# Performance work log

Measured on AMD Instinct MI355X. Metric: run time of the kernel, lower is better.

## Reference

```python
import jax, jax.numpy as jnp
import numpy as np

N_NODES = 100000
N_EDGES = 400000
N_GRAPHS = 4096
IN_DIM = 128
HID = 64
HEADS = 8
NEG_SLOPE = 0.2


def setup_inputs() -> dict:
    key = jax.random.key(0)
    ks = jax.random.split(key, 12)
    x = jax.random.normal(ks[0], (N_NODES, IN_DIM), dtype=jnp.float32)
    edge_index = jax.random.randint(ks[1], (2, N_EDGES), 0, N_NODES, dtype=jnp.int64)
    batch = jnp.sort(jax.random.randint(ks[2], (N_NODES,), 0, N_GRAPHS, dtype=jnp.int64))
    s = 1.0 / np.sqrt(IN_DIM)
    W1 = jax.random.normal(ks[3], (IN_DIM, HEADS * HID), dtype=jnp.float32) * s
    att_src1 = jax.random.normal(ks[4], (HEADS, HID), dtype=jnp.float32) * 0.1
    att_dst1 = jax.random.normal(ks[5], (HEADS, HID), dtype=jnp.float32) * 0.1
    b1 = jnp.zeros((HEADS * HID,), dtype=jnp.float32)
    s2 = 1.0 / np.sqrt(HEADS * HID)
    W2 = jax.random.normal(ks[6], (HEADS * HID, HID), dtype=jnp.float32) * s2
    att_src2 = jax.random.normal(ks[7], (1, HID), dtype=jnp.float32) * 0.1
    att_dst2 = jax.random.normal(ks[8], (1, HID), dtype=jnp.float32) * 0.1
    b2 = jnp.zeros((HID,), dtype=jnp.float32)
    Wf = jax.random.normal(ks[9], (HID, 1), dtype=jnp.float32) * (1.0 / np.sqrt(HID))
    bf = jnp.zeros((1,), dtype=jnp.float32)
    return {"x": x, "edge_index": edge_index, "batch": batch,
            "W1": W1, "att_src1": att_src1, "att_dst1": att_dst1, "b1": b1,
            "W2": W2, "att_src2": att_src2, "att_dst2": att_dst2, "b2": b2,
            "Wf": Wf, "bf": bf}


def _gat_layer(x, src, dst, W, att_src, att_dst, bias, heads, out_ch, concat):
    # PyG GATConv math (add_self_loops handled by caller via src/dst)
    n = x.shape[0]
    h = (x @ W).reshape(n, heads, out_ch)          # [N, H, C]
    a_s = (h * att_src[None]).sum(-1)               # [N, H]
    a_d = (h * att_dst[None]).sum(-1)               # [N, H]
    alpha = a_s[src] + a_d[dst]                     # [E, H]
    alpha = jax.nn.leaky_relu(alpha, NEG_SLOPE)
    amax = jax.ops.segment_max(alpha, dst, num_segments=n)
    alpha = jnp.exp(alpha - amax[dst])
    denom = jax.ops.segment_sum(alpha, dst, num_segments=n)
    alpha = alpha / (denom[dst] + 1e-16)
    msg = h[src] * alpha[:, :, None]                # [E, H, C]
    out = jax.ops.segment_sum(msg, dst, num_segments=n)  # [N, H, C]
    out = out.reshape(n, heads * out_ch) if concat else out.mean(axis=1)
    return out + bias


def reference(x, edge_index, batch, W1, att_src1, att_dst1, b1,
              W2, att_src2, att_dst2, b2, Wf, bf):
    n = x.shape[0]
    loop = jnp.arange(n, dtype=edge_index.dtype)
    src = jnp.concatenate([edge_index[0], loop])
    dst = jnp.concatenate([edge_index[1], loop])
    h = _gat_layer(x, src, dst, W1, att_src1, att_dst1, b1, HEADS, HID, True)
    h = jax.nn.relu(h)
    h = _gat_layer(h, src, dst, W2, att_src2, att_dst2, b2, 1, HID, False)
    h = jax.nn.relu(h)
    sums = jax.ops.segment_sum(h, batch, num_segments=N_GRAPHS)        # [G, HID]
    cnts = jax.ops.segment_sum(jnp.ones((n,), h.dtype), batch, num_segments=N_GRAPHS)
    pooled = sums / jnp.clip(cnts, 1.0)[:, None]
    return pooled @ Wf + bf
```

## Files before the change

### kernel.cpp

```cpp
#include <hip/hip_runtime.h>

typedef short bfrag8 __attribute__((ext_vector_type(8)));
typedef float f32x4 __attribute__((ext_vector_type(4)));
typedef unsigned int uint4v __attribute__((ext_vector_type(4)));

#define SCAN_BLK 2048

__device__ __forceinline__ unsigned short f2bf(float f) {
    unsigned u = __float_as_uint(f);
    u += 0x7fffu + ((u >> 16) & 1u);
    return (unsigned short)(u >> 16);
}
__device__ __forceinline__ float bf2f(unsigned short s) {
    return __uint_as_float((unsigned)s << 16);
}

__global__ __launch_bounds__(256) void prologue(const float* __restrict__ x,
                                                unsigned short* __restrict__ x_bf,
                                                int* __restrict__ cnt,
                                                const float* __restrict__ W1,
                                                const float* __restrict__ W2,
                                                unsigned short* __restrict__ wf1,
                                                unsigned short* __restrict__ wf2,
                                                const int* __restrict__ batch,
                                                int* __restrict__ gstart,
                                                int* __restrict__ rs,
                                                int N, int G, int E) {
    const int b = blockIdx.x, t = threadIdx.x;
    if (b < 1024) {
        size_t n = (size_t)N * 128;
        size_t i = ((size_t)b * 256 + t) * 4;
        size_t stride = 1024llu * 256 * 4;
        for (; i < n; i += stride) {
            float4 v = *(const float4*)(x + i);
            x_bf[i + 0] = f2bf(v.x);
            x_bf[i + 1] = f2bf(v.y);
            x_bf[i + 2] = f2bf(v.z);
            x_bf[i + 3] = f2bf(v.w);
        }
    } else if (b < 1536) {
        int i = (b - 1024) * 256 + t;
        if (i < N) cnt[i] = 0;
    } else if (b < 1792) {
        int i = (b - 1536) * 256 + t;
        if (i < 8 * 4 * 4 * 64 * 8) {
            int e = i & 7, l = (i >> 3) & 63, c = (i >> 9) & 3, s = (i >> 11) & 3, h = i >> 13;
            int k = s * 32 + (l >> 4) * 8 + e;
            int col = h * 64 + c * 16 + (l & 15);
            wf1[i] = f2bf(W1[k * 512 + col]);
        }
    } else if (b < 1920) {
        int i = (b - 1792) * 256 + t;
        if (i < 16 * 4 * 64 * 8) {
            int e = i & 7, l = (i >> 3) & 63, c = (i >> 9) & 3, s = i >> 11;
            int k = s * 32 + (l >> 4) * 8 + e;
            int col = c * 16 + (l & 15);
            wf2[i] = f2bf(W2[k * 64 + col]);
        }
    } else {
        int i = (b - 1920) * 256 + t;
        if (i == 0) rs[N] = E + N;
        if (i > N) return;
        if (i == N) {
            int p = batch[N - 1];
            for (int g = p + 1; g <= G; ++g) gstart[g] = N;
        } else {
            int bb = batch[i];
            int p = (i == 0) ? -1 : batch[i - 1];
            for (int g = p + 1; g <= bb; ++g) gstart[g] = i;
        }
    }
}

__global__ __launch_bounds__(256) void gemm_l1_hist(const unsigned short* __restrict__ A,
                                                    const unsigned short* __restrict__ Bfrag,
                                                    unsigned short* __restrict__ Cbf,
                                                    int M,
                                                    const float* __restrict__ avs,
                                                    const float* __restrict__ avd,
                                                    float* __restrict__ as_,
                                                    float* __restrict__ ad_,
                                                    int gemmBlocks, int rowBlocks,
                                                    const int* __restrict__ ei,
                                                    int* __restrict__ cnt, int E) {
    const int b = blockIdx.x;
    if (b >= gemmBlocks) {
        int t = (b - gemmBlocks) * 256 + threadIdx.x;
        if (t < E + M) {
            int dst = (t < E) ? ei[E + t] : t - E;
            atomicAdd(cnt + dst, 1);
        }
        return;
    }
    const int rb = b % rowBlocks;
    const int cb = b / rowBlocks;
    const int lane = threadIdx.x & 63;
    const int wave = threadIdx.x >> 6;
    const int l15 = lane & 15, l16 = lane >> 4;
    const long rowBase = (long)rb * 128 + wave * 32;

    bfrag8 bf[4][4];
    const bfrag8* bp = (const bfrag8*)(Bfrag + (size_t)cb * 8192);
#pragma unroll
    for (int s = 0; s < 4; ++s)
#pragma unroll
        for (int c = 0; c < 4; ++c)
            bf[s][c] = bp[(s * 4 + c) * 64 + lane];

    f32x4 acc[2][4];
#pragma unroll
    for (int r = 0; r < 2; ++r)
#pragma unroll
        for (int c = 0; c < 4; ++c)
#pragma unroll
            for (int e = 0; e < 4; ++e) acc[r][c][e] = 0.f;

    long r0 = rowBase + l15;        if (r0 > M - 1) r0 = M - 1;
    long r1 = rowBase + 16 + l15;   if (r1 > M - 1) r1 = M - 1;
    const unsigned short* a0p = A + r0 * 128 + l16 * 8;
    const unsigned short* a1p = A + r1 * 128 + l16 * 8;

#pragma unroll
    for (int s = 0; s < 4; ++s) {
        bfrag8 a0 = *(const bfrag8*)(a0p + s * 32);
        bfrag8 a1 = *(const bfrag8*)(a1p + s * 32);
#pragma unroll
        for (int c = 0; c < 4; ++c) {
            acc[0][c] = __builtin_amdgcn_mfma_f32_16x16x32_bf16(a0, bf[s][c], acc[0][c], 0, 0, 0);
            acc[1][c] = __builtin_amdgcn_mfma_f32_16x16x32_bf16(a1, bf[s][c], acc[1][c], 0, 0, 0);
        }
    }

    float avsv[4], avdv[4];
#pragma unroll
    for (int c = 0; c < 4; ++c) {
        avsv[c] = avs[cb * 64 + c * 16 + l15];
        avdv[c] = avd[cb * 64 + c * 16 + l15];
    }

#pragma unroll
    for (int r = 0; r < 2; ++r) {
#pragma unroll
        for (int reg = 0; reg < 4; ++reg) {
            long row = rowBase + r * 16 + l16 * 4 + reg;
            bool ok = row < M;
            float ps = 0.f, pd = 0.f;
#pragma unroll
            for (int c = 0; c < 4; ++c) {
                float v = acc[r][c][reg];
                if (ok) Cbf[row * 512 + cb * 64 + c * 16 + l15] = f2bf(v);
                ps += v * avsv[c];
                pd += v * avdv[c];
            }
#pragma unroll
            for (int off = 1; off < 16; off <<= 1) {
                ps += __shfl_xor(ps, off);
                pd += __shfl_xor(pd, off);
            }
            if (l15 == 0 && ok) {
                as_[row * 8 + cb] = ps;
                ad_[row * 8 + cb] = pd;
            }
        }
    }
}

__global__ __launch_bounds__(256) void scan1(const int* __restrict__ cnt,
                                             int* __restrict__ rs,
                                             int* __restrict__ bsum, int N) {
    __shared__ int lds[256];
    int base = blockIdx.x * SCAN_BLK;
    int vals[8];
    int tsum = 0;
    int idx0 = base + threadIdx.x * 8;
#pragma unroll
    for (int j = 0; j < 8; ++j) {
        int i = idx0 + j;
        int v = (i < N) ? cnt[i] : 0;
        vals[j] = tsum;
        tsum += v;
    }
    lds[threadIdx.x] = tsum;
    __syncthreads();
    for (int off = 1; off < 256; off <<= 1) {
        int v = lds[threadIdx.x];
        int u = (threadIdx.x >= (unsigned)off) ? lds[threadIdx.x - off] : 0;
        __syncthreads();
        lds[threadIdx.x] = v + u;
        __syncthreads();
    }
    int texcl = (threadIdx.x == 0) ? 0 : lds[threadIdx.x - 1];
#pragma unroll
    for (int j = 0; j < 8; ++j) {
        int i = idx0 + j;
        if (i < N) rs[i] = texcl + vals[j];
    }
    if (threadIdx.x == 255) bsum[blockIdx.x] = lds[255];
}

__global__ __launch_bounds__(256) void scan_fix(int* __restrict__ rs,
                                                const int* __restrict__ bsum, int N) {
    __shared__ int sprefix;
    int b = blockIdx.x;
    int i = b * 256 + threadIdx.x;
    int chunk = (b * 256) / SCAN_BLK;
    if (threadIdx.x == 0) {
        int p = 0;
        for (int k = 0; k < chunk; ++k) p += bsum[k];
        sprefix = p;
    }
    __syncthreads();
    if (i < N) rs[i] += sprefix;
}

__global__ __launch_bounds__(256) void scatter_cd(const int* __restrict__ ei,
                                                  const int* __restrict__ rs,
                                                  int* __restrict__ cnt,
                                                  int* __restrict__ csrc, int E, int N) {
    int t = (int)(blockIdx.x * 256u + threadIdx.x);
    if (t >= E + N) return;
    int src, dst;
    if (t < E) { src = ei[t]; dst = ei[E + t]; } else { src = dst = t - E; }
    int pos = rs[dst] + atomicSub(cnt + dst, 1) - 1;
    csrc[pos] = src;
}

__global__ __launch_bounds__(256) void gather8(const int* __restrict__ csrc,
                                               const int* __restrict__ rs,
                                               const float* __restrict__ as_,
                                               const float* __restrict__ ad_,
                                               const unsigned short* __restrict__ h,
                                               const float* __restrict__ bias,
                                               unsigned short* __restrict__ outp,
                                               int N) {
    int node = (int)((blockIdx.x * 256u + threadIdx.x) >> 6);
    int lane = threadIdx.x & 63;
    if (node >= N) return;
    int myh = lane >> 3;
    int s0 = rs[node], s1 = rs[node + 1];
    float adn = ad_[(size_t)node * 8 + myh];
    float den = 0.f;
    float2 acc[4] = {};
    const unsigned* hu = (const unsigned*)h;
    int k = s0;
    for (; k + 4 <= s1; k += 4) {
        int i0 = csrc[k], i1 = csrc[k + 1], i2 = csrc[k + 2], i3 = csrc[k + 3];
        float a0 = as_[(size_t)i0 * 8 + myh] + adn;
        float a1 = as_[(size_t)i1 * 8 + myh] + adn;
        float a2 = as_[(size_t)i2 * 8 + myh] + adn;
        float a3 = as_[(size_t)i3 * 8 + myh] + adn;
        a0 = a0 > 0.f ? a0 : 0.2f * a0;  a1 = a1 > 0.f ? a1 : 0.2f * a1;
        a2 = a2 > 0.f ? a2 : 0.2f * a2;  a3 = a3 > 0.f ? a3 : 0.2f * a3;
        float w0 = __expf(fminf(a0, 60.f)), w1 = __expf(fminf(a1, 60.f));
        float w2 = __expf(fminf(a2, 60.f)), w3 = __expf(fminf(a3, 60.f));
        uint4v v0 = *(const uint4v*)(hu + (size_t)i0 * 256 + lane * 4);
        uint4v v1 = *(const uint4v*)(hu + (size_t)i1 * 256 + lane * 4);
        uint4v v2 = *(const uint4v*)(hu + (size_t)i2 * 256 + lane * 4);
        uint4v v3 = *(const uint4v*)(hu + (size_t)i3 * 256 + lane * 4);
        den += (w0 + w1) + (w2 + w3);
#pragma unroll
        for (int j = 0; j < 4; ++j) {
            acc[j].x += w0 * __uint_as_float(v0[j] << 16);
            acc[j].y += w0 * __uint_as_float(v0[j] & 0xffff0000u);
            acc[j].x += w1 * __uint_as_float(v1[j] << 16);
            acc[j].y += w1 * __uint_as_float(v1[j] & 0xffff0000u);
            acc[j].x += w2 * __uint_as_float(v2[j] << 16);
            acc[j].y += w2 * __uint_as_float(v2[j] & 0xffff0000u);
            acc[j].x += w3 * __uint_as_float(v3[j] << 16);
            acc[j].y += w3 * __uint_as_float(v3[j] & 0xffff0000u);
        }
    }
    for (; k < s1; ++k) {
        int i0 = csrc[k];
        float a = as_[(size_t)i0 * 8 + myh] + adn;
        a = a > 0.f ? a : 0.2f * a;
        float w = __expf(fminf(a, 60.f));
        uint4v v0 = *(const uint4v*)(hu + (size_t)i0 * 256 + lane * 4);
        den += w;
#pragma unroll
        for (int j = 0; j < 4; ++j) {
            acc[j].x += w * __uint_as_float(v0[j] << 16);
            acc[j].y += w * __uint_as_float(v0[j] & 0xffff0000u);
        }
    }
    float rden = 1.f / (den + 1e-16f);
    uint4v o;
#pragma unroll
    for (int j = 0; j < 4; ++j) {
        float vlo = acc[j].x * rden + bias[lane * 8 + 2 * j];
        float vhi = acc[j].y * rden + bias[lane * 8 + 2 * j + 1];
        vlo = vlo > 0.f ? vlo : 0.f;
        vhi = vhi > 0.f ? vhi : 0.f;
        o[j] = (unsigned)f2bf(vlo) | ((unsigned)f2bf(vhi) << 16);
    }
    *(uint4v*)(outp + (size_t)node * 512 + lane * 8) = o;
}

__global__ __launch_bounds__(256) void gemm_l2_k512(const unsigned short* __restrict__ A,
                                                    const unsigned short* __restrict__ Bfrag,
                                                    unsigned short* __restrict__ Cbf,
                                                    int M,
                                                    const float* __restrict__ avs,
                                                    const float* __restrict__ avd,
                                                    float* __restrict__ as_,
                                                    float* __restrict__ ad_) {
    const int lane = threadIdx.x & 63;
    const int wave = threadIdx.x >> 6;
    const int l15 = lane & 15, l16 = lane >> 4;
    const long rowBase = (long)blockIdx.x * 128 + wave * 32;
    const bfrag8* bp = (const bfrag8*)Bfrag;

    f32x4 acc[2][4];
#pragma unroll
    for (int r = 0; r < 2; ++r)
#pragma unroll
        for (int c = 0; c < 4; ++c)
#pragma unroll
            for (int e = 0; e < 4; ++e) acc[r][c][e] = 0.f;

    long r0 = rowBase + l15;        if (r0 > M - 1) r0 = M - 1;
    long r1 = rowBase + 16 + l15;   if (r1 > M - 1) r1 = M - 1;
    const unsigned short* a0p = A + r0 * 512 + l16 * 8;
    const unsigned short* a1p = A + r1 * 512 + l16 * 8;

    for (int s = 0; s < 16; ++s) {
        bfrag8 a0 = *(const bfrag8*)(a0p + s * 32);
        bfrag8 a1 = *(const bfrag8*)(a1p + s * 32);
        bfrag8 bf0 = bp[(s * 4 + 0) * 64 + lane];
        bfrag8 bf1 = bp[(s * 4 + 1) * 64 + lane];
        bfrag8 bf2 = bp[(s * 4 + 2) * 64 + lane];
        bfrag8 bf3 = bp[(s * 4 + 3) * 64 + lane];
        acc[0][0] = __builtin_amdgcn_mfma_f32_16x16x32_bf16(a0, bf0, acc[0][0], 0, 0, 0);
        acc[1][0] = __builtin_amdgcn_mfma_f32_16x16x32_bf16(a1, bf0, acc[1][0], 0, 0, 0);
        acc[0][1] = __builtin_amdgcn_mfma_f32_16x16x32_bf16(a0, bf1, acc[0][1], 0, 0, 0);
        acc[1][1] = __builtin_amdgcn_mfma_f32_16x16x32_bf16(a1, bf1, acc[1][1], 0, 0, 0);
        acc[0][2] = __builtin_amdgcn_mfma_f32_16x16x32_bf16(a0, bf2, acc[0][2], 0, 0, 0);
        acc[1][2] = __builtin_amdgcn_mfma_f32_16x16x32_bf16(a1, bf2, acc[1][2], 0, 0, 0);
        acc[0][3] = __builtin_amdgcn_mfma_f32_16x16x32_bf16(a0, bf3, acc[0][3], 0, 0, 0);
        acc[1][3] = __builtin_amdgcn_mfma_f32_16x16x32_bf16(a1, bf3, acc[1][3], 0, 0, 0);
    }

    float avsv[4], avdv[4];
#pragma unroll
    for (int c = 0; c < 4; ++c) {
        avsv[c] = avs[c * 16 + l15];
        avdv[c] = avd[c * 16 + l15];
    }

#pragma unroll
    for (int r = 0; r < 2; ++r) {
#pragma unroll
        for (int reg = 0; reg < 4; ++reg) {
            long row = rowBase + r * 16 + l16 * 4 + reg;
            bool ok = row < M;
            float ps = 0.f, pd = 0.f;
#pragma unroll
            for (int c = 0; c < 4; ++c) {
                float v = acc[r][c][reg];
                if (ok) Cbf[row * 64 + c * 16 + l15] = f2bf(v);
                ps += v * avsv[c];
                pd += v * avdv[c];
            }
#pragma unroll
            for (int off = 1; off < 16; off <<= 1) {
                ps += __shfl_xor(ps, off);
                pd += __shfl_xor(pd, off);
            }
            if (l15 == 0 && ok) { as_[row] = ps; ad_[row] = pd; }
        }
    }
}

__global__ __launch_bounds__(256) void gather1(const int* __restrict__ csrc,
                                               const int* __restrict__ rs,
                                               const float* __restrict__ as_,
                                               const float* __restrict__ ad_,
                                               const unsigned short* __restrict__ h,
                                               const float* __restrict__ bias,
                                               float* __restrict__ outp, int N) {
    int node = (int)((blockIdx.x * 256u + threadIdx.x) >> 6);
    int lane = threadIdx.x & 63;
    if (node >= N) return;
    int s0 = rs[node], s1 = rs[node + 1];
    float adn = ad_[node];
    float den = 0.f, acc = 0.f;
    int k = s0;
    for (; k + 4 <= s1; k += 4) {
        int i0 = csrc[k], i1 = csrc[k + 1], i2 = csrc[k + 2], i3 = csrc[k + 3];
        float a0 = as_[i0] + adn, a1 = as_[i1] + adn, a2 = as_[i2] + adn, a3 = as_[i3] + adn;
        a0 = a0 > 0.f ? a0 : 0.2f * a0;  a1 = a1 > 0.f ? a1 : 0.2f * a1;
        a2 = a2 > 0.f ? a2 : 0.2f * a2;  a3 = a3 > 0.f ? a3 : 0.2f * a3;
        float w0 = __expf(fminf(a0, 60.f)), w1 = __expf(fminf(a1, 60.f));
        float w2 = __expf(fminf(a2, 60.f)), w3 = __expf(fminf(a3, 60.f));
        float h0 = bf2f(h[(size_t)i0 * 64 + lane]);
        float h1 = bf2f(h[(size_t)i1 * 64 + lane]);
        float h2 = bf2f(h[(size_t)i2 * 64 + lane]);
        float h3 = bf2f(h[(size_t)i3 * 64 + lane]);
        den += (w0 + w1) + (w2 + w3);
        acc += w0 * h0;  acc += w1 * h1;  acc += w2 * h2;  acc += w3 * h3;
    }
    for (; k < s1; ++k) {
        int i0 = csrc[k];
        float a = as_[i0] + adn;
        a = a > 0.f ? a : 0.2f * a;
        float w = __expf(fminf(a, 60.f));
        den += w;
        acc += w * bf2f(h[(size_t)i0 * 64 + lane]);
    }
    float v = acc / (den + 1e-16f) + bias[lane];
    outp[(size_t)node * 64 + lane] = v > 0.f ? v : 0.f;
}

__global__ __launch_bounds__(256) void pool_readout(const float* __restrict__ h2,
                                                    const int* __restrict__ gstart,
                                                    const float* __restrict__ Wf,
                                                    const float* __restrict__ bf,
                                                    float* __restrict__ out, int G) {
    int g = (int)((blockIdx.x * 256u + threadIdx.x) >> 6);
    int lane = threadIdx.x & 63;
    if (g >= G) return;
    int s0 = gstart[g], s1 = gstart[g + 1];
    float acc = 0.f;
    int i = s0;
    for (; i + 2 <= s1; i += 2) {
        acc += h2[(size_t)i * 64 + lane];
        acc += h2[(size_t)(i + 1) * 64 + lane];
    }
    if (i < s1) acc += h2[(size_t)i * 64 + lane];
    float c = (float)(s1 - s0);
    c = c < 1.f ? 1.f : c;
    float v = acc / c * Wf[lane];
#pragma unroll
    for (int off = 32; off; off >>= 1) v += __shfl_xor(v, off);
    if (lane == 0) out[g] = v + bf[0];
}

extern "C" void kernel_launch(void* const* d_in, const int* in_sizes, int n_in,
                              void* d_out, int out_size, void* d_ws, size_t ws_size,
                              hipStream_t stream) {
    const float* x        = (const float*)d_in[0];
    const int*   ei       = (const int*)d_in[1];
    const int*   batch    = (const int*)d_in[2];
    const float* W1       = (const float*)d_in[3];
    const float* att_src1 = (const float*)d_in[4];
    const float* att_dst1 = (const float*)d_in[5];
    const float* b1       = (const float*)d_in[6];
    const float* W2       = (const float*)d_in[7];
    const float* att_src2 = (const float*)d_in[8];
    const float* att_dst2 = (const float*)d_in[9];
    const float* b2       = (const float*)d_in[10];
    const float* Wf       = (const float*)d_in[11];
    const float* bf       = (const float*)d_in[12];
    float* out = (float*)d_out;

    const int N = in_sizes[2];
    const int E = in_sizes[1] / 2;
    const int G = out_size;

    const int nb = (N + SCAN_BLK - 1) / SCAN_BLK;
    const int nodeWaveGrid = (int)(((size_t)N * 64 + 255) / 256);
    const int edgeGrid = (E + N + 255) / 256;
    const int gemmGrid = (N + 127) / 128;

    char* base = (char*)d_ws;
    size_t off = 0;
    auto alloc = [&](size_t bytes) { char* p = base + off; off += (bytes + 255) & ~255llu; return p; };
    unsigned short* wf1   = (unsigned short*)alloc(131072);
    unsigned short* wf2   = (unsigned short*)alloc(65536);
    float* as1            = (float*)alloc((size_t)N * 8 * 4);
    float* ad1            = (float*)alloc((size_t)N * 8 * 4);
    float* as2            = (float*)alloc((size_t)N * 4);
    float* ad2            = (float*)alloc((size_t)N * 4);
    int*   cnt_i          = (int*)alloc((size_t)N * 4);
    int*   rs             = (int*)alloc((size_t)(N + 1) * 4);
    int*   csrc           = (int*)alloc((size_t)(E + N) * 4);
    int*   bsum           = (int*)alloc(1024);
    int*   gstart         = (int*)alloc((size_t)(G + 1) * 4);
    unsigned short* x_bf  = (unsigned short*)alloc((size_t)N * 128 * 2);
    float* ob2            = (float*)x_bf;
    unsigned short* h2bf  = (unsigned short*)alloc((size_t)N * 64 * 2);
    unsigned short* h1_bf = (unsigned short*)alloc((size_t)N * 512 * 2);
    unsigned short* ob1_bf= (unsigned short*)alloc((size_t)N * 512 * 2);
    (void)ws_size;

    {
        int gsBlocks = (N + 256) / 256 + 1;
        int grid = 1920 + gsBlocks;
        prologue<<<grid, 256, 0, stream>>>(x, x_bf, cnt_i, W1, W2, wf1, wf2,
                                           batch, gstart, rs, N, G, E);
    }

    {
        int gemmBlocks = gemmGrid * 8;
        gemm_l1_hist<<<gemmBlocks + edgeGrid, 256, 0, stream>>>(
            x_bf, wf1, h1_bf, N, att_src1, att_dst1, as1, ad1,
            gemmBlocks, gemmGrid, ei, cnt_i, E);
    }

    scan1<<<nb, 256, 0, stream>>>(cnt_i, rs, bsum, N);
    scan_fix<<<(N + 255) / 256, 256, 0, stream>>>(rs, bsum, N);
    scatter_cd<<<edgeGrid, 256, 0, stream>>>(ei, rs, cnt_i, csrc, E, N);

    gather8<<<nodeWaveGrid, 256, 0, stream>>>(csrc, rs, as1, ad1, h1_bf, b1, ob1_bf, N);

    gemm_l2_k512<<<gemmGrid, 256, 0, stream>>>(ob1_bf, wf2, h2bf, N,
                                               att_src2, att_dst2, as2, ad2);

    gather1<<<nodeWaveGrid, 256, 0, stream>>>(csrc, rs, as2, ad2, h2bf, b2, ob2, N);

    pool_readout<<<(G * 64 + 255) / 256, 256, 0, stream>>>(ob2, gstart, Wf, bf, out, G);
}
```

Baseline: 292.7 us.

## Fuse fp32-to-bf16 input conversion into layer-1 GEMM and loop heads per block

The prologue no longer converts x to bf16. The layer-1 GEMM now reads fp32 x directly, packs it to bf16 fragments in registers once, and loops over all 8 heads inside one block, so each A row is loaded only once rather than once per head-block. This removes an N×128 bf16 write and read and the 8x re-reading of A. The cost is fewer GEMM blocks, which lowers parallelism and adds per-block serial work. The gather kernels also replace the scalar remainder loop with a masked 4-wide tail that reuses index s0 for padded slots.

After: 282.4 us. -3.5%, faster.

```diff
diff --git a/kernel.cpp b/kernel.cpp
--- a/kernel.cpp
+++ b/kernel.cpp
@@ -14,10 +14,16 @@
 __device__ __forceinline__ float bf2f(unsigned short s) {
     return __uint_as_float((unsigned)s << 16);
 }
-
-__global__ __launch_bounds__(256) void prologue(const float* __restrict__ x,
-                                                unsigned short* __restrict__ x_bf,
-                                                int* __restrict__ cnt,
+__device__ __forceinline__ bfrag8 pack8(float4 a, float4 b) {
+    bfrag8 r;
+    r[0] = (short)f2bf(a.x); r[1] = (short)f2bf(a.y);
+    r[2] = (short)f2bf(a.z); r[3] = (short)f2bf(a.w);
+    r[4] = (short)f2bf(b.x); r[5] = (short)f2bf(b.y);
+    r[6] = (short)f2bf(b.z); r[7] = (short)f2bf(b.w);
+    return r;
+}
+
+__global__ __launch_bounds__(256) void prologue(int* __restrict__ cnt,
                                                 const float* __restrict__ W1,
                                                 const float* __restrict__ W2,
                                                 unsigned short* __restrict__ wf1,
@@ -27,38 +33,23 @@
                                                 int* __restrict__ rs,
                                                 int N, int G, int E) {
     const int b = blockIdx.x, t = threadIdx.x;
-    if (b < 1024) {
-        size_t n = (size_t)N * 128;
-        size_t i = ((size_t)b * 256 + t) * 4;
-        size_t stride = 1024llu * 256 * 4;
-        for (; i < n; i += stride) {
-            float4 v = *(const float4*)(x + i);
-            x_bf[i + 0] = f2bf(v.x);
-            x_bf[i + 1] = f2bf(v.y);
-            x_bf[i + 2] = f2bf(v.z);
-            x_bf[i + 3] = f2bf(v.w);
-        }
-    } else if (b < 1536) {
-        int i = (b - 1024) * 256 + t;
+    if (b < 512) {
+        int i = b * 256 + t;
         if (i < N) cnt[i] = 0;
-    } else if (b < 1792) {
-        int i = (b - 1536) * 256 + t;
-        if (i < 8 * 4 * 4 * 64 * 8) {
-            int e = i & 7, l = (i >> 3) & 63, c = (i >> 9) & 3, s = (i >> 11) & 3, h = i >> 13;
-            int k = s * 32 + (l >> 4) * 8 + e;
-            int col = h * 64 + c * 16 + (l & 15);
-            wf1[i] = f2bf(W1[k * 512 + col]);
-        }
-    } else if (b < 1920) {
-        int i = (b - 1792) * 256 + t;
-        if (i < 16 * 4 * 64 * 8) {
-            int e = i & 7, l = (i >> 3) & 63, c = (i >> 9) & 3, s = i >> 11;
-            int k = s * 32 + (l >> 4) * 8 + e;
-            int col = c * 16 + (l & 15);
-            wf2[i] = f2bf(W2[k * 64 + col]);
-        }
+    } else if (b < 768) {
+        int i = (b - 512) * 256 + t;
+        int e = i & 7, l = (i >> 3) & 63, c = (i >> 9) & 3, s = (i >> 11) & 3, h = i >> 13;
+        int k = s * 32 + (l >> 4) * 8 + e;
+        int col = h * 64 + c * 16 + (l & 15);
+        wf1[i] = f2bf(W1[k * 512 + col]);
+    } else if (b < 896) {
+        int i = (b - 768) * 256 + t;
+        int e = i & 7, l = (i >> 3) & 63, c = (i >> 9) & 3, s = i >> 11;
+        int k = s * 32 + (l >> 4) * 8 + e;
+        int col = c * 16 + (l & 15);
+        wf2[i] = f2bf(W2[k * 64 + col]);
     } else {
-        int i = (b - 1920) * 256 + t;
+        int i = (b - 896) * 256 + t;
         if (i == 0) rs[N] = E + N;
         if (i > N) return;
         if (i == N) {
@@ -72,7 +63,7 @@
     }
 }
 
-__global__ __launch_bounds__(256) void gemm_l1_hist(const unsigned short* __restrict__ A,
+__global__ __launch_bounds__(256) void gemm_l1_hist(const float* __restrict__ x,
                                                     const unsigned short* __restrict__ Bfrag,
                                                     unsigned short* __restrict__ Cbf,
                                                     int M,
@@ -80,7 +71,7 @@
                                                     const float* __restrict__ avd,
                                                     float* __restrict__ as_,
                                                     float* __restrict__ ad_,
-                                                    int gemmBlocks, int rowBlocks,
+                                                    int gemmBlocks,
                                                     const int* __restrict__ ei,
                                                     int* __restrict__ cnt, int E) {
     const int b = blockIdx.x;
@@ -92,74 +83,82 @@
         }
         return;
     }
-    const int rb = b % rowBlocks;
-    const int cb = b / rowBlocks;
     const int lane = threadIdx.x & 63;
     const int wave = threadIdx.x >> 6;
     const int l15 = lane & 15, l16 = lane >> 4;
-    const long rowBase = (long)rb * 128 + wave * 32;
-
-    bfrag8 bf[4][4];
-    const bfrag8* bp = (const bfrag8*)(Bfrag + (size_t)cb * 8192);
-#pragma unroll
-    for (int s = 0; s < 4; ++s)
-#pragma unroll
-        for (int c = 0; c < 4; ++c)
-            bf[s][c] = bp[(s * 4 + c) * 64 + lane];
-
-    f32x4 acc[2][4];
-#pragma unroll
-    for (int r = 0; r < 2; ++r)
-#pragma unroll
-        for (int c = 0; c < 4; ++c)
-#pragma unroll
-            for (int e = 0; e < 4; ++e) acc[r][c][e] = 0.f;
+    const long rowBase = (long)b * 128 + wave * 32;
 
     long r0 = rowBase + l15;        if (r0 > M - 1) r0 = M - 1;
     long r1 = rowBase + 16 + l15;   if (r1 > M - 1) r1 = M - 1;
-    const unsigned short* a0p = A + r0 * 128 + l16 * 8;
-    const unsigned short* a1p = A + r1 * 128 + l16 * 8;
-
+
+    bfrag8 a0f[4], a1f[4];
 #pragma unroll
     for (int s = 0; s < 4; ++s) {
-        bfrag8 a0 = *(const bfrag8*)(a0p + s * 32);
-        bfrag8 a1 = *(const bfrag8*)(a1p + s * 32);
+        const float* p0 = x + r0 * 128 + s * 32 + l16 * 8;
+        const float* p1 = x + r1 * 128 + s * 32 + l16 * 8;
+        float4 u0 = *(const float4*)p0, u1 = *(const float4*)(p0 + 4);
+        float4 v0 = *(const float4*)p1, v1 = *(const float4*)(p1 + 4);
+        a0f[s] = pack8(u0, u1);
+        a1f[s] = pack8(v0, v1);
+    }
+
+#pragma unroll 1
+    for (int h = 0; h < 8; ++h) {
+        bfrag8 bf[4][4];
+        const bfrag8* bp = (const bfrag8*)(Bfrag + (size_t)h * 8192);
+#pragma unroll
+        for (int s = 0; s < 4; ++s)
+#pragma unroll
+            for (int c = 0; c < 4; ++c)
+                bf[s][c] = bp[(s * 4 + c) * 64 + lane];
+
+        f32x4 acc[2][4];
+#pragma unroll
+        for (int r = 0; r < 2; ++r)
+#pragma unroll
+            for (int c = 0; c < 4; ++c)
+#pragma unroll
+                for (int e = 0; e < 4; ++e) acc[r][c][e] = 0.f;
+
+#pragma unroll
+        for (int s = 0; s < 4; ++s) {
+#pragma unroll
+            for (int c = 0; c < 4; ++c) {
+                acc[0][c] = __builtin_amdgcn_mfma_f32_16x16x32_bf16(a0f[s], bf[s][c], acc[0][c], 0, 0, 0);
+                acc[1][c] = __builtin_amdgcn_mfma_f32_16x16x32_bf16(a1f[s], bf[s][c], acc[1][c], 0, 0, 0);
+            }
+        }
+
+        float avsv[4], avdv[4];
 #pragma unroll
         for (int c = 0; c < 4; ++c) {
-            acc[0][c] = __builtin_amdgcn_mfma_f32_16x16x32_bf16(a0, bf[s][c], acc[0][c], 0, 0, 0);
-            acc[1][c] = __builtin_amdgcn_mfma_f32_16x16x32_bf16(a1, bf[s][c], acc[1][c], 0, 0, 0);
-        }
-    }
-
-    float avsv[4], avdv[4];
-#pragma unroll
-    for (int c = 0; c < 4; ++c) {
-        avsv[c] = avs[cb * 64 + c * 16 + l15];
-        avdv[c] = avd[cb * 64 + c * 16 + l15];
-    }
-
-#pragma unroll
-    for (int r = 0; r < 2; ++r) {
-#pragma unroll
-        for (int reg = 0; reg < 4; ++reg) {
-            long row = rowBase + r * 16 + l16 * 4 + reg;
-            bool ok = row < M;
-            float ps = 0.f, pd = 0.f;
-#pragma unroll
-            for (int c = 0; c < 4; ++c) {
-                float v = acc[r][c][reg];
-                if (ok) Cbf[row * 512 + cb * 64 + c * 16 + l15] = f2bf(v);
-                ps += v * avsv[c];
-                pd += v * avdv[c];
-            }
-#pragma unroll
-            for (int off = 1; off < 16; off <<= 1) {
-                ps += __shfl_xor(ps, off);
-                pd += __shfl_xor(pd, off);
-            }
-            if (l15 == 0 && ok) {
-                as_[row * 8 + cb] = ps;
-                ad_[row * 8 + cb] = pd;
+            avsv[c] = avs[h * 64 + c * 16 + l15];
+            avdv[c] = avd[h * 64 + c * 16 + l15];
+        }
+
+#pragma unroll
+        for (int r = 0; r < 2; ++r) {
+#pragma unroll
+            for (int reg = 0; reg < 4; ++reg) {
+                long row = rowBase + r * 16 + l16 * 4 + reg;
+                bool ok = row < M;
+                float ps = 0.f, pd = 0.f;
+#pragma unroll
+                for (int c = 0; c < 4; ++c) {
+                    float v = acc[r][c][reg];
+                    if (ok) Cbf[row * 512 + h * 64 + c * 16 + l15] = f2bf(v);
+                    ps += v * avsv[c];
+                    pd += v * avdv[c];
+                }
+#pragma unroll
+                for (int off = 1; off < 16; off <<= 1) {
+                    ps += __shfl_xor(ps, off);
+                    pd += __shfl_xor(pd, off);
+                }
+                if (l15 == 0 && ok) {
+                    as_[row * 8 + h] = ps;
+                    ad_[row * 8 + h] = pd;
+                }
             }
         }
     }
@@ -242,17 +241,22 @@
     float den = 0.f;
     float2 acc[4] = {};
     const unsigned* hu = (const unsigned*)h;
-    int k = s0;
-    for (; k + 4 <= s1; k += 4) {
-        int i0 = csrc[k], i1 = csrc[k + 1], i2 = csrc[k + 2], i3 = csrc[k + 3];
+    for (int k = s0; k < s1; k += 4) {
+        int k1 = k + 1 < s1 ? k + 1 : s0;
+        int k2 = k + 2 < s1 ? k + 2 : s0;
+        int k3 = k + 3 < s1 ? k + 3 : s0;
+        bool m1 = k + 1 < s1, m2 = k + 2 < s1, m3 = k + 3 < s1;
+        int i0 = csrc[k], i1 = csrc[k1], i2 = csrc[k2], i3 = csrc[k3];
         float a0 = as_[(size_t)i0 * 8 + myh] + adn;
         float a1 = as_[(size_t)i1 * 8 + myh] + adn;
         float a2 = as_[(size_t)i2 * 8 + myh] + adn;
         float a3 = as_[(size_t)i3 * 8 + myh] + adn;
         a0 = a0 > 0.f ? a0 : 0.2f * a0;  a1 = a1 > 0.f ? a1 : 0.2f * a1;
         a2 = a2 > 0.f ? a2 : 0.2f * a2;  a3 = a3 > 0.f ? a3 : 0.2f * a3;
-        float w0 = __expf(fminf(a0, 60.f)), w1 = __expf(fminf(a1, 60.f));
-        float w2 = __expf(fminf(a2, 60.f)), w3 = __expf(fminf(a3, 60.f));
+        float w0 = __expf(fminf(a0, 60.f));
+        float w1 = m1 ? __expf(fminf(a1, 60.f)) : 0.f;
+        float w2 = m2 ? __expf(fminf(a2, 60.f)) : 0.f;
+        float w3 = m3 ? __expf(fminf(a3, 60.f)) : 0.f;
         uint4v v0 = *(const uint4v*)(hu + (size_t)i0 * 256 + lane * 4);
         uint4v v1 = *(const uint4v*)(hu + (size_t)i1 * 256 + lane * 4);
         uint4v v2 = *(const uint4v*)(hu + (size_t)i2 * 256 + lane * 4);
@@ -268,19 +272,6 @@
             acc[j].y += w2 * __uint_as_float(v2[j] & 0xffff0000u);
             acc[j].x += w3 * __uint_as_float(v3[j] << 16);
             acc[j].y += w3 * __uint_as_float(v3[j] & 0xffff0000u);
-        }
-    }
-    for (; k < s1; ++k) {
-        int i0 = csrc[k];
-        float a = as_[(size_t)i0 * 8 + myh] + adn;
-        a = a > 0.f ? a : 0.2f * a;
-        float w = __expf(fminf(a, 60.f));
-        uint4v v0 = *(const uint4v*)(hu + (size_t)i0 * 256 + lane * 4);
-        den += w;
-#pragma unroll
-        for (int j = 0; j < 4; ++j) {
-            acc[j].x += w * __uint_as_float(v0[j] << 16);
-            acc[j].y += w * __uint_as_float(v0[j] & 0xffff0000u);
         }
     }
     float rden = 1.f / (den + 1e-16f);
@@ -384,28 +375,25 @@
     int s0 = rs[node], s1 = rs[node + 1];
     float adn = ad_[node];
     float den = 0.f, acc = 0.f;
-    int k = s0;
-    for (; k + 4 <= s1; k += 4) {
-        int i0 = csrc[k], i1 = csrc[k + 1], i2 = csrc[k + 2], i3 = csrc[k + 3];
+    for (int k = s0; k < s1; k += 4) {
+        int k1 = k + 1 < s1 ? k + 1 : s0;
+        int k2 = k + 2 < s1 ? k + 2 : s0;
+        int k3 = k + 3 < s1 ? k + 3 : s0;
+        bool m1 = k + 1 < s1, m2 = k + 2 < s1, m3 = k + 3 < s1;
+        int i0 = csrc[k], i1 = csrc[k1], i2 = csrc[k2], i3 = csrc[k3];
         float a0 = as_[i0] + adn, a1 = as_[i1] + adn, a2 = as_[i2] + adn, a3 = as_[i3] + adn;
         a0 = a0 > 0.f ? a0 : 0.2f * a0;  a1 = a1 > 0.f ? a1 : 0.2f * a1;
         a2 = a2 > 0.f ? a2 : 0.2f * a2;  a3 = a3 > 0.f ? a3 : 0.2f * a3;
-        float w0 = __expf(fminf(a0, 60.f)), w1 = __expf(fminf(a1, 60.f));
-        float w2 = __expf(fminf(a2, 60.f)), w3 = __expf(fminf(a3, 60.f));
+        float w0 = __expf(fminf(a0, 60.f));
+        float w1 = m1 ? __expf(fminf(a1, 60.f)) : 0.f;
+        float w2 = m2 ? __expf(fminf(a2, 60.f)) : 0.f;
+        float w3 = m3 ? __expf(fminf(a3, 60.f)) : 0.f;
         float h0 = bf2f(h[(size_t)i0 * 64 + lane]);
         float h1 = bf2f(h[(size_t)i1 * 64 + lane]);
         float h2 = bf2f(h[(size_t)i2 * 64 + lane]);
         float h3 = bf2f(h[(size_t)i3 * 64 + lane]);
         den += (w0 + w1) + (w2 + w3);
         acc += w0 * h0;  acc += w1 * h1;  acc += w2 * h2;  acc += w3 * h3;
-    }
-    for (; k < s1; ++k) {
-        int i0 = csrc[k];
-        float a = as_[i0] + adn;
-        a = a > 0.f ? a : 0.2f * a;
-        float w = __expf(fminf(a, 60.f));
-        den += w;
-        acc += w * bf2f(h[(size_t)i0 * 64 + lane]);
     }
     float v = acc / (den + 1e-16f) + bias[lane];
     outp[(size_t)node * 64 + lane] = v > 0.f ? v : 0.f;
@@ -476,8 +464,7 @@
     int*   csrc           = (int*)alloc((size_t)(E + N) * 4);
     int*   bsum           = (int*)alloc(1024);
     int*   gstart         = (int*)alloc((size_t)(G + 1) * 4);
-    unsigned short* x_bf  = (unsigned short*)alloc((size_t)N * 128 * 2);
-    float* ob2            = (float*)x_bf;
+    float* ob2            = (float*)alloc((size_t)N * 64 * 4);
     unsigned short* h2bf  = (unsigned short*)alloc((size_t)N * 64 * 2);
     unsigned short* h1_bf = (unsigned short*)alloc((size_t)N * 512 * 2);
     unsigned short* ob1_bf= (unsigned short*)alloc((size_t)N * 512 * 2);
@@ -485,17 +472,13 @@
 
     {
         int gsBlocks = (N + 256) / 256 + 1;
-        int grid = 1920 + gsBlocks;
-        prologue<<<grid, 256, 0, stream>>>(x, x_bf, cnt_i, W1, W2, wf1, wf2,
-                                           batch, gstart, rs, N, G, E);
-    }
-
-    {
-        int gemmBlocks = gemmGrid * 8;
-        gemm_l1_hist<<<gemmBlocks + edgeGrid, 256, 0, stream>>>(
-            x_bf, wf1, h1_bf, N, att_src1, att_dst1, as1, ad1,
-            gemmBlocks, gemmGrid, ei, cnt_i, E);
-    }
+        prologue<<<896 + gsBlocks, 256, 0, stream>>>(cnt_i, W1, W2, wf1, wf2,
+                                                     batch, gstart, rs, N, G, E);
+    }
+
+    gemm_l1_hist<<<gemmGrid + edgeGrid, 256, 0, stream>>>(
+        x, wf1, h1_bf, N, att_src1, att_dst1, as1, ad1,
+        gemmGrid, ei, cnt_i, E);
 
     scan1<<<nb, 256, 0, stream>>>(cnt_i, rs, bsum, N);
     scan_fix<<<(N + 255) / 256, 256, 0, stream>>>(rs, bsum, N);
```
